# Performance work log

Measured on AMD Instinct MI355X. Metric: run time of the kernel, lower is better.

## Reference

```python
import jax, jax.numpy as jnp
import numpy as np

B, K, D, FD = 4096, 200, 128, 1024  # batch, neighbors, embed dim, item_fields*D
MASK_FILL = -(2.0 ** 32) + 1.0


def setup_inputs() -> dict:
    key = jax.random.key(0)
    k1, k2, k3, k4, k5 = jax.random.split(key, 5)
    target_feats = jax.random.normal(k1, (B, FD), dtype=jnp.float32)
    neighbor_feats = jax.random.normal(k2, (B, K, D), dtype=jnp.float32)
    neighbor_label = jax.random.normal(k3, (B, K, D), dtype=jnp.float32)
    hist_mask = jax.random.randint(k4, (B, K), 0, 2, dtype=jnp.int32)
    # Linear(item_fields*D -> D, bias=False): weight shape (out, in) = (D, FD)
    limit = float(np.sqrt(6.0 / (D + FD)))  # xavier_uniform
    W = jax.random.uniform(k5, (D, FD), dtype=jnp.float32, minval=-limit, maxval=limit)
    return {"target_feats": target_feats, "neighbor_feats": neighbor_feats,
            "neighbor_label": neighbor_label, "hist_mask": hist_mask, "W": W}


def reference(target_feats, neighbor_feats, neighbor_label, hist_mask, W):
    # target = self.W(target_feats): [B, D]
    target = jnp.einsum('bf,df->bd', target_feats, W)
    # alpha = matmul(neighbor_feats, target[..., None]).squeeze(): [B, K]
    alpha = jnp.einsum('bkd,bd->bk', neighbor_feats, target)
    alpha = jnp.where(hist_mask > 0, alpha, MASK_FILL)
    alpha = jax.nn.softmax(alpha, axis=1)  # [B, K]
    neighbor_embd = jnp.einsum('bk,bkd->bd', alpha, neighbor_feats)
    label_embd = jnp.einsum('bk,bkd->bd', alpha, neighbor_label)
    return (neighbor_embd, label_embd)
```

## Files before the change

### kernel.cpp

```cpp
#include <hip/hip_runtime.h>
#include <math.h>

#define BB   4096
#define KK   200
#define DD   128
#define FDIM 1024
#define MASK_FILL (-4294967295.0f)

typedef float fx4 __attribute__((ext_vector_type(4)));

__device__ __forceinline__ float red32(float v) {
    #pragma unroll
    for (int off = 16; off > 0; off >>= 1) v += __shfl_xor(v, off);
    return v;
}

__global__ __launch_bounds__(256) void target_gemm(const float* __restrict__ tf,
                                                   const float* __restrict__ W,
                                                   float* __restrict__ tgt) {
    __shared__ float s_tf[8 * FDIM];
    __shared__ float s_red[8][DD];
    const int tid = threadIdx.x;
    const int d   = tid & 127;
    const int h   = tid >> 7;
    const size_t r0 = (size_t)blockIdx.x * 8;

    const fx4* src = (const fx4*)(tf + r0 * FDIM);
    for (int i = tid; i < 8 * FDIM / 4; i += 256)
        ((fx4*)s_tf)[i] = src[i];
    __syncthreads();

    float acc[8] = {0, 0, 0, 0, 0, 0, 0, 0};
    const fx4* wr = (const fx4*)(W + (size_t)d * FDIM) + h * (FDIM / 8);
    #pragma unroll 4
    for (int i = 0; i < FDIM / 8; ++i) {
        fx4 w = wr[i];
        #pragma unroll
        for (int r = 0; r < 8; ++r) {
            fx4 t = ((const fx4*)(s_tf + r * FDIM + h * (FDIM / 2)))[i];
            acc[r] += w.x * t.x + w.y * t.y + w.z * t.z + w.w * t.w;
        }
    }
    if (h == 1) {
        #pragma unroll
        for (int r = 0; r < 8; ++r) s_red[r][d] = acc[r];
    }
    __syncthreads();
    if (h == 0) {
        #pragma unroll
        for (int r = 0; r < 8; ++r)
            tgt[(r0 + r) * DD + d] = acc[r] + s_red[r][d];
    }
}

__global__ __launch_bounds__(256, 8) void attn_online(const float* __restrict__ nf,
                                                      const float* __restrict__ nl,
                                                      const int*   __restrict__ mask,
                                                      const float* __restrict__ tgt,
                                                      float* __restrict__ out) {
    __shared__ float s_m[2][2], s_s[2][2];
    __shared__ fx4   s_an[2][2][32];
    __shared__ fx4   s_al[2][2][32];

    const int tid  = threadIdx.x;
    const int lane = tid & 63;
    const int l32  = lane & 31;
    const int h    = (lane >> 5) & 1;
    const int bloc = tid >> 7;
    const int b    = __builtin_amdgcn_readfirstlane(blockIdx.x * 2 + bloc);
    const int w    = __builtin_amdgcn_readfirstlane((tid >> 6) & 1);

    const fx4* nf4 = (const fx4*)(nf + (size_t)b * KK * DD) + (size_t)w * 50 * 64;
    const fx4* nl4 = (const fx4*)(nl + (size_t)b * KK * DD) + (size_t)w * 50 * 64;
    const int* mb  = mask + (size_t)b * KK + w * 100;
    const fx4  tg  = ((const fx4*)(tgt + (size_t)b * DD))[l32];

    float m = -INFINITY, s = 0.0f;
    fx4 an = {0, 0, 0, 0}, al = {0, 0, 0, 0};

#define LOADC(N0, N1, L0, L1, c)                                    \
    {                                                               \
        const int base_ = (c) * 128 + lane;                         \
        N0 = __builtin_nontemporal_load(nf4 + base_);               \
        N1 = __builtin_nontemporal_load(nf4 + base_ + 64);          \
        L0 = __builtin_nontemporal_load(nl4 + base_);               \
        L1 = __builtin_nontemporal_load(nl4 + base_ + 64);          \
    }

#define COMPC(N0, N1, L0, L1, c)                                             \
    {                                                                        \
        float a0 = red32(N0.x * tg.x + N0.y * tg.y + N0.z * tg.z + N0.w * tg.w); \
        float a1 = red32(N1.x * tg.x + N1.y * tg.y + N1.z * tg.z + N1.w * tg.w); \
        const int k0_ = (c) * 4;                                             \
        const int mA_ = h ? mb[k0_ + 1] : mb[k0_];                           \
        const int mB_ = h ? mb[k0_ + 3] : mb[k0_ + 2];                       \
        a0 = (mA_ > 0) ? a0 : MASK_FILL;                                     \
        a1 = (mB_ > 0) ? a1 : MASK_FILL;                                     \
        const float mn_ = fmaxf(m, fmaxf(a0, a1));                           \
        const float r_  = __expf(m - mn_);                                   \
        m = mn_;                                                             \
        s *= r_; an *= r_; al *= r_;                                         \
        const float p0_ = __expf(a0 - m);                                    \
        const float p1_ = __expf(a1 - m);                                    \
        s += p0_ + p1_;                                                      \
        an += p0_ * N0 + p1_ * N1;                                           \
        al += p0_ * L0 + p1_ * L1;                                           \
    }

    fx4 nA0, nA1, lA0, lA1, nB0, nB1, lB0, lB1;
    LOADC(nA0, nA1, lA0, lA1, 0)
    for (int c = 0; c < 24; c += 2) {
        LOADC(nB0, nB1, lB0, lB1, c + 1)
        COMPC(nA0, nA1, lA0, lA1, c)
        LOADC(nA0, nA1, lA0, lA1, c + 2)
        COMPC(nB0, nB1, lB0, lB1, c + 1)
    }
    COMPC(nA0, nA1, lA0, lA1, 24)

#undef LOADC
#undef COMPC

    {
        const float mo = __shfl_xor(m, 32);
        const float so = __shfl_xor(s, 32);
        fx4 ano, alo;
        ano.x = __shfl_xor(an.x, 32); ano.y = __shfl_xor(an.y, 32);
        ano.z = __shfl_xor(an.z, 32); ano.w = __shfl_xor(an.w, 32);
        alo.x = __shfl_xor(al.x, 32); alo.y = __shfl_xor(al.y, 32);
        alo.z = __shfl_xor(al.z, 32); alo.w = __shfl_xor(al.w, 32);
        const float mt = fmaxf(m, mo);
        const float e0 = __expf(m - mt);
        const float e1 = __expf(mo - mt);
        s  = s * e0 + so * e1;
        an = an * e0 + ano * e1;
        al = al * e0 + alo * e1;
        m  = mt;
    }

    if (h == 0) s_an[bloc][w][l32] = an; else s_al[bloc][w][l32] = al;
    if (lane == 0) { s_m[bloc][w] = m; s_s[bloc][w] = s; }
    __syncthreads();

    if (w == 0) {
        const float m1 = s_m[bloc][1];
        const float s1 = s_s[bloc][1];
        const fx4 mine  = (h == 0) ? an : al;
        const fx4 other = (h == 0) ? s_an[bloc][1][l32] : s_al[bloc][1][l32];
        const float M   = fmaxf(m, m1);
        const float e0  = __expf(m - M);
        const float e1  = __expf(m1 - M);
        const float inv = 1.0f / (s * e0 + s1 * e1);
        const fx4 r = (mine * e0 + other * e1) * inv;
        if (h == 0)
            __builtin_nontemporal_store(r, &((fx4*)(out + (size_t)b * DD))[l32]);
        else
            __builtin_nontemporal_store(r, &((fx4*)(out + (size_t)BB * DD + (size_t)b * DD))[l32]);
    }
}

extern "C" void kernel_launch(void* const* d_in, const int* in_sizes, int n_in,
                              void* d_out, int out_size, void* d_ws, size_t ws_size,
                              hipStream_t stream) {
    const float* tf   = (const float*)d_in[0];
    const float* nf   = (const float*)d_in[1];
    const float* nl   = (const float*)d_in[2];
    const int*   mask = (const int*)d_in[3];
    const float* W    = (const float*)d_in[4];
    float* out = (float*)d_out;
    float* tgt = (float*)d_ws;

    target_gemm<<<BB / 8, 256, 0, stream>>>(tf, W, tgt);
    attn_online<<<BB / 2, 256, 0, stream>>>(nf, nl, mask, tgt, out);
}
```

Before: 173.0 us.

## Fuse target GEMM and attention into one kernel with flag-based producer sync

```diff
diff --git a/kernel.cpp b/kernel.cpp
--- a/kernel.cpp
+++ b/kernel.cpp
@@ -6,6 +6,7 @@
 #define DD   128
 #define FDIM 1024
 #define MASK_FILL (-4294967295.0f)
+#define NPROD 512
 
 typedef float fx4 __attribute__((ext_vector_type(4)));
 
@@ -15,68 +16,63 @@
     return v;
 }
 
-__global__ __launch_bounds__(256) void target_gemm(const float* __restrict__ tf,
-                                                   const float* __restrict__ W,
-                                                   float* __restrict__ tgt) {
-    __shared__ float s_tf[8 * FDIM];
+__global__ __launch_bounds__(256, 8) void fused(const float* __restrict__ tf,
+                                                const float* __restrict__ nf,
+                                                const float* __restrict__ nl,
+                                                const int*   __restrict__ mask,
+                                                const float* __restrict__ W,
+                                                float* __restrict__ tgt,
+                                                int*   __restrict__ flags,
+                                                float* __restrict__ out) {
     __shared__ float s_red[8][DD];
-    const int tid = threadIdx.x;
-    const int d   = tid & 127;
-    const int h   = tid >> 7;
-    const size_t r0 = (size_t)blockIdx.x * 8;
-
-    const fx4* src = (const fx4*)(tf + r0 * FDIM);
-    for (int i = tid; i < 8 * FDIM / 4; i += 256)
-        ((fx4*)s_tf)[i] = src[i];
-    __syncthreads();
-
-    float acc[8] = {0, 0, 0, 0, 0, 0, 0, 0};
-    const fx4* wr = (const fx4*)(W + (size_t)d * FDIM) + h * (FDIM / 8);
-    #pragma unroll 4
-    for (int i = 0; i < FDIM / 8; ++i) {
-        fx4 w = wr[i];
-        #pragma unroll
-        for (int r = 0; r < 8; ++r) {
-            fx4 t = ((const fx4*)(s_tf + r * FDIM + h * (FDIM / 2)))[i];
-            acc[r] += w.x * t.x + w.y * t.y + w.z * t.z + w.w * t.w;
-        }
-    }
-    if (h == 1) {
-        #pragma unroll
-        for (int r = 0; r < 8; ++r) s_red[r][d] = acc[r];
-    }
-    __syncthreads();
-    if (h == 0) {
-        #pragma unroll
-        for (int r = 0; r < 8; ++r)
-            tgt[(r0 + r) * DD + d] = acc[r] + s_red[r][d];
-    }
-}
-
-__global__ __launch_bounds__(256, 8) void attn_online(const float* __restrict__ nf,
-                                                      const float* __restrict__ nl,
-                                                      const int*   __restrict__ mask,
-                                                      const float* __restrict__ tgt,
-                                                      float* __restrict__ out) {
     __shared__ float s_m[2][2], s_s[2][2];
     __shared__ fx4   s_an[2][2][32];
     __shared__ fx4   s_al[2][2][32];
 
-    const int tid  = threadIdx.x;
+    const int tid = threadIdx.x;
+    const int bid = blockIdx.x;
+
+    if (bid < NPROD) {
+        const int d = tid & 127;
+        const int h = tid >> 7;
+        const size_t r0 = (size_t)bid * 8;
+        const fx4* wr  = (const fx4*)(W + (size_t)d * FDIM) + h * (FDIM / 8);
+        const fx4* tf4 = (const fx4*)(tf + r0 * FDIM) + h * (FDIM / 8);
+        float acc[8] = {0, 0, 0, 0, 0, 0, 0, 0};
+        #pragma unroll 4
+        for (int i = 0; i < FDIM / 8; ++i) {
+            const fx4 w = wr[i];
+            #pragma unroll
+            for (int r = 0; r < 8; ++r) {
+                const fx4 t = tf4[r * (FDIM / 4) + i];
+                acc[r] += w.x * t.x + w.y * t.y + w.z * t.z + w.w * t.w;
+            }
+        }
+        if (h == 1) {
+            #pragma unroll
+            for (int r = 0; r < 8; ++r) s_red[r][d] = acc[r];
+        }
+        __syncthreads();
+        if (h == 0) {
+            #pragma unroll
+            for (int r = 0; r < 8; ++r)
+                tgt[(r0 + r) * DD + d] = acc[r] + s_red[r][d];
+        }
+        __syncthreads();
+        if (tid == 0)
+            __hip_atomic_store(flags + bid, 1, __ATOMIC_RELEASE, __HIP_MEMORY_SCOPE_AGENT);
+    }
+
     const int lane = tid & 63;
     const int l32  = lane & 31;
-    const int h    = (lane >> 5) & 1;
+    const int h2   = (lane >> 5) & 1;
     const int bloc = tid >> 7;
-    const int b    = __builtin_amdgcn_readfirstlane(blockIdx.x * 2 + bloc);
-    const int w    = __builtin_amdgcn_readfirstlane((tid >> 6) & 1);
+    const int b    = __builtin_amdgcn_readfirstlane(bid * 2 + bloc);
+    const int kw   = __builtin_amdgcn_readfirstlane((tid >> 6) & 1);
 
-    const fx4* nf4 = (const fx4*)(nf + (size_t)b * KK * DD) + (size_t)w * 50 * 64;
-    const fx4* nl4 = (const fx4*)(nl + (size_t)b * KK * DD) + (size_t)w * 50 * 64;
-    const int* mb  = mask + (size_t)b * KK + w * 100;
-    const fx4  tg  = ((const fx4*)(tgt + (size_t)b * DD))[l32];
-
-    float m = -INFINITY, s = 0.0f;
-    fx4 an = {0, 0, 0, 0}, al = {0, 0, 0, 0};
+    const fx4* nf4 = (const fx4*)(nf + (size_t)b * KK * DD) + (size_t)kw * 50 * 64;
+    const fx4* nl4 = (const fx4*)(nl + (size_t)b * KK * DD) + (size_t)kw * 50 * 64;
+    const int* mb  = mask + (size_t)b * KK + kw * 100;
 
 #define LOADC(N0, N1, L0, L1, c)                                    \
     {                                                               \
@@ -92,8 +88,8 @@
         float a0 = red32(N0.x * tg.x + N0.y * tg.y + N0.z * tg.z + N0.w * tg.w); \
         float a1 = red32(N1.x * tg.x + N1.y * tg.y + N1.z * tg.z + N1.w * tg.w); \
         const int k0_ = (c) * 4;                                             \
-        const int mA_ = h ? mb[k0_ + 1] : mb[k0_];                           \
-        const int mB_ = h ? mb[k0_ + 3] : mb[k0_ + 2];                       \
+        const int mA_ = h2 ? mb[k0_ + 1] : mb[k0_];                          \
+        const int mB_ = h2 ? mb[k0_ + 3] : mb[k0_ + 2];                      \
         a0 = (mA_ > 0) ? a0 : MASK_FILL;                                     \
         a1 = (mB_ > 0) ? a1 : MASK_FILL;                                     \
         const float mn_ = fmaxf(m, fmaxf(a0, a1));                           \
@@ -109,6 +105,21 @@
 
     fx4 nA0, nA1, lA0, lA1, nB0, nB1, lB0, lB1;
     LOADC(nA0, nA1, lA0, lA1, 0)
+
+    if (tid == 0) {
+        while (__hip_atomic_load(flags + (b >> 3), __ATOMIC_RELAXED,
+                                 __HIP_MEMORY_SCOPE_AGENT) == 0)
+            __builtin_amdgcn_s_sleep(8);
+    }
+    __syncthreads();
+    __builtin_amdgcn_fence(__ATOMIC_ACQUIRE, "agent");
+    __builtin_amdgcn_sched_barrier(0);
+
+    const fx4 tg = ((const fx4*)(tgt + (size_t)b * DD))[l32];
+
+    float m = -INFINITY, s = 0.0f;
+    fx4 an = {0, 0, 0, 0}, al = {0, 0, 0, 0};
+
     for (int c = 0; c < 24; c += 2) {
         LOADC(nB0, nB1, lB0, lB1, c + 1)
         COMPC(nA0, nA1, lA0, lA1, c)
@@ -137,21 +148,21 @@
         m  = mt;
     }
 
-    if (h == 0) s_an[bloc][w][l32] = an; else s_al[bloc][w][l32] = al;
-    if (lane == 0) { s_m[bloc][w] = m; s_s[bloc][w] = s; }
+    if (h2 == 0) s_an[bloc][kw][l32] = an; else s_al[bloc][kw][l32] = al;
+    if (lane == 0) { s_m[bloc][kw] = m; s_s[bloc][kw] = s; }
     __syncthreads();
 
-    if (w == 0) {
+    if (kw == 0) {
         const float m1 = s_m[bloc][1];
         const float s1 = s_s[bloc][1];
-        const fx4 mine  = (h == 0) ? an : al;
-        const fx4 other = (h == 0) ? s_an[bloc][1][l32] : s_al[bloc][1][l32];
+        const fx4 mine  = (h2 == 0) ? an : al;
+        const fx4 other = (h2 == 0) ? s_an[bloc][1][l32] : s_al[bloc][1][l32];
         const float M   = fmaxf(m, m1);
         const float e0  = __expf(m - M);
         const float e1  = __expf(m1 - M);
         const float inv = 1.0f / (s * e0 + s1 * e1);
         const fx4 r = (mine * e0 + other * e1) * inv;
-        if (h == 0)
+        if (h2 == 0)
             __builtin_nontemporal_store(r, &((fx4*)(out + (size_t)b * DD))[l32]);
         else
             __builtin_nontemporal_store(r, &((fx4*)(out + (size_t)BB * DD + (size_t)b * DD))[l32]);
@@ -166,9 +177,10 @@
     const float* nl   = (const float*)d_in[2];
     const int*   mask = (const int*)d_in[3];
     const float* W    = (const float*)d_in[4];
-    float* out = (float*)d_out;
-    float* tgt = (float*)d_ws;
+    float* out   = (float*)d_out;
+    float* tgt   = (float*)d_ws;
+    int*   flags = (int*)((char*)d_ws + 2 * 1024 * 1024);
 
-    target_gemm<<<BB / 8, 256, 0, stream>>>(tf, W, tgt);
-    attn_online<<<BB / 2, 256, 0, stream>>>(nf, nl, mask, tgt, out);
+    hipMemsetAsync(flags, 0, NPROD * sizeof(int), stream);
+    fused<<<BB / 2, 256, 0, stream>>>(tf, nf, nl, mask, W, tgt, flags, out);
 }
```

New measurement: 410.6 us. +137.4%, slower.
